# Performance work log

Hardware: AMD Instinct MI355X
Metric: run time of the kernel (lower is better)

## Reference

```python
import jax, jax.numpy as jnp
import numpy as np

B, N, D, L, V, E = 16, 512, 512, 4, 128, 131072
PAD = 127

def setup_inputs() -> dict:
    key = jax.random.key(0)
    ks = jax.random.split(key, 16)
    src_tokens = jax.random.randint(ks[0], (B, N), 0, PAD)  # 0..126, never PAD
    padded_coordinates = jax.random.normal(ks[1], (B, N, 3), dtype=jnp.float32)
    src_distance = jax.random.uniform(ks[2], (B, N, N), dtype=jnp.float32)
    src_edge_type = jax.random.randint(ks[3], (B, N, N), 0, 16)
    edge_index = jax.random.randint(ks[4], (2, E), 0, B * N)
    s = 0.02
    embed_tokens = jax.random.normal(ks[5], (V, D), dtype=jnp.float32) * s
    embed_tokens = embed_tokens.at[PAD].set(0.0)  # nn.Embedding padding_idx row is zero
    vec_proj_w = jax.random.normal(ks[6], (3, D), dtype=jnp.float32) * s
    vec_proj_b = jnp.zeros((D,), dtype=jnp.float32)
    Wq = jax.random.normal(ks[7], (L, D, D), dtype=jnp.float32) * s
    bq = jnp.zeros((L, D), dtype=jnp.float32)
    Wkv = jax.random.normal(ks[8], (L, D, 3 * D), dtype=jnp.float32) * s
    bkv = jnp.zeros((L, 3 * D), dtype=jnp.float32)
    Wvm = jax.random.normal(ks[9], (L, D, D), dtype=jnp.float32) * s
    bvm = jnp.zeros((L, D), dtype=jnp.float32)
    return dict(src_tokens=src_tokens, padded_coordinates=padded_coordinates,
                src_distance=src_distance, src_edge_type=src_edge_type,
                edge_index=edge_index, embed_tokens=embed_tokens,
                vec_proj_w=vec_proj_w, vec_proj_b=vec_proj_b,
                Wq=Wq, bq=bq, Wkv=Wkv, bkv=bkv, Wvm=Wvm, bvm=bvm)

def reference(src_tokens, padded_coordinates, src_distance, src_edge_type,
              edge_index, embed_tokens, vec_proj_w, vec_proj_b,
              Wq, bq, Wkv, bkv, Wvm, bvm):
    padding_mask = src_tokens == PAD                      # [B,N] (all False here)
    x = embed_tokens[src_tokens].reshape(B * N, D)        # [BN,D]
    coord = padded_coordinates.reshape(B * N, 3)          # [BN,3]
    v = coord @ vec_proj_w + vec_proj_b                   # [BN,D]
    row, col = edge_index[0], edge_index[1]               # [E]
    for l in range(L):
        q = x @ Wq[l] + bq[l]                             # [BN,D]
        kv = x @ Wkv[l] + bkv[l]                          # [BN,3D]
        k, v_s, v_v = jnp.split(kv, 3, axis=-1)
        ew = jnp.sum(q[row] * k[col], axis=-1, keepdims=True)   # [E,1] edge score
        msg_s = ew * v_s[col]                             # [E,D]
        msg_v = ew * v_v[col] * v[col]                    # [E,D] gated vector message
        agg_s = jnp.zeros_like(x).at[row].add(msg_s)      # scatter-add to dest nodes
        agg_v = jnp.zeros_like(v).at[row].add(msg_v)
        x = x + agg_s
        v = v + (agg_v @ Wvm[l] + bvm[l])
    out = jnp.where(padding_mask.reshape(-1, 1), 0.0, x).reshape(B, N, D)
    return out, padding_mask
```

## Files before the change

kernel.cpp:

```cpp
#include <hip/hip_runtime.h>
#include <hip/hip_bf16.h>

#define NNODE 8192
#define DIM 512
#define NEDGE 131072
#define NLAYER 4
#define PADIDX 127

typedef float4 f4;
typedef __attribute__((ext_vector_type(8))) short s16x8;
typedef __attribute__((ext_vector_type(4))) float f32x4;

static __device__ __forceinline__ float bf2f(unsigned short h){
  return __uint_as_float(((unsigned int)h) << 16);
}
static __device__ __forceinline__ unsigned short f2bf(float f){
  unsigned int u = __float_as_uint(f);
  u += 0x7FFFu + ((u >> 16) & 1u);
  return (unsigned short)(u >> 16);
}
static __device__ __forceinline__ float blo(unsigned int u){ return __uint_as_float(u << 16); }
static __device__ __forceinline__ float bhi(unsigned int u){ return __uint_as_float(u & 0xFFFF0000u); }
static __device__ __forceinline__ unsigned int pack2(float a, float b){
  return (unsigned int)f2bf(a) | ((unsigned int)f2bf(b) << 16);
}

__global__ void k_detect(const unsigned short* __restrict__ src, int* __restrict__ flag){
  int lane = threadIdx.x;
  float v = bf2f(src[2*lane]);
  float a = fabsf(v);
  bool good = (a > 1e-6f) && (a < 0.5f);
  unsigned long long m = __ballot(good);
  if (lane == 0) *flag = (__popcll(m) >= 32) ? 1 : 0;
}

__global__ void k_convert(const void* __restrict__ src, float* __restrict__ dst, int n,
                          const int* __restrict__ flag){
  int f = *flag;
  int i = blockIdx.x*blockDim.x + threadIdx.x;
  int stride = gridDim.x*blockDim.x;
  if (f){
    const unsigned short* s = (const unsigned short*)src;
    for (; i<n; i+=stride) dst[i] = bf2f(s[i]);
  } else {
    const float* s = (const float*)src;
    for (; i<n; i+=stride) dst[i] = s[i];
  }
}

__global__ void k_convT(const void* __restrict__ src, unsigned short* __restrict__ dst,
                        int C, int dstOff, int dstStride, const int* __restrict__ flag){
  int f = *flag;
  int i = blockIdx.x*blockDim.x + threadIdx.x;
  if (i >= 512*C) return;
  int r = i & 511;
  int c = i >> 9;
  size_t si = (size_t)blockIdx.z*512*C + (size_t)r*C + c;
  unsigned short o;
  if (f) o = ((const unsigned short*)src)[si];
  else   o = f2bf(((const float*)src)[si]);
  dst[(size_t)blockIdx.z*dstStride + (size_t)(dstOff + c)*512 + r] = o;
}

__global__ void k_bias(const void* __restrict__ bq, const void* __restrict__ bkv,
                       float* __restrict__ dst, const int* __restrict__ flag){
  int f = *flag;
  int gid = blockIdx.x*blockDim.x + threadIdx.x;
  if (gid >= NLAYER*2048) return;
  int l = gid >> 11, j = gid & 2047;
  float val;
  if (j < 512)
    val = f ? bf2f(((const unsigned short*)bq)[l*512+j]) : ((const float*)bq)[l*512+j];
  else
    val = f ? bf2f(((const unsigned short*)bkv)[l*1536 + j-512]) : ((const float*)bkv)[l*1536 + j-512];
  dst[gid] = val;
}

__global__ void k_zero_i(int* __restrict__ p, int n){
  int i = blockIdx.x*blockDim.x + threadIdx.x;
  if (i<n) p[i]=0;
}

__global__ void k_count(const int* __restrict__ row, int* __restrict__ counts){
  int e = blockIdx.x*blockDim.x + threadIdx.x;
  if (e<NEDGE) atomicAdd(&counts[row[e]], 1);
}

__global__ __launch_bounds__(1024) void k_scan(const int* __restrict__ counts,
                                               int* __restrict__ offs, int* __restrict__ cursor){
  __shared__ int part[1024];
  int tid = threadIdx.x;
  int local[8]; int s = 0;
  #pragma unroll
  for (int j=0;j<8;j++){ local[j]=s; s += counts[tid*8+j]; }
  part[tid]=s;
  __syncthreads();
  for (int off=1; off<1024; off<<=1){
    int t = (tid>=off) ? part[tid-off] : 0;
    __syncthreads();
    part[tid] += t;
    __syncthreads();
  }
  int base = (tid>0) ? part[tid-1] : 0;
  #pragma unroll
  for (int j=0;j<8;j++){ int o = base + local[j]; offs[tid*8+j]=o; cursor[tid*8+j]=o; }
  if (tid==1023) offs[8192] = part[1023];
}

__global__ void k_fill(const int* __restrict__ ei, int* __restrict__ cursor, int* __restrict__ ecol){
  int e = blockIdx.x*blockDim.x + threadIdx.x;
  if (e<NEDGE){ int p = atomicAdd(&cursor[ei[e]], 1); ecol[p] = ei[NEDGE+e]; }
}

__global__ void k_init(const int* __restrict__ tok, const float* __restrict__ emb,
                       const float* __restrict__ coord, const float* __restrict__ vw,
                       const float* __restrict__ vb, float* __restrict__ x,
                       float* __restrict__ v, unsigned short* __restrict__ xbf){
  int i = blockIdx.x*blockDim.x + threadIdx.x;
  if (i >= NNODE*DIM) return;
  int n = i >> 9, d = i & 511;
  int t = tok[n];
  float xv = emb[(t<<9)|d];
  x[i] = xv;
  xbf[i] = f2bf(xv);
  float c0 = coord[n*3+0], c1 = coord[n*3+1], c2 = coord[n*3+2];
  v[i] = c0*vw[d] + c1*vw[512+d] + c2*vw[1024+d] + vb[d];
}

#define BM 128
#define BN 128
#define BK 64

static __device__ __forceinline__ void gload16(const void* g, void* l){
  __builtin_amdgcn_global_load_lds(
      (const __attribute__((address_space(1))) void*)g,
      (__attribute__((address_space(3))) void*)l, 16, 0, 0);
}

__global__ __launch_bounds__(256) void k_mgemm(const unsigned short* __restrict__ A,
                                               const unsigned short* __restrict__ Bt,
                                               const float* __restrict__ bias,
                                               void* __restrict__ C,
                                               int ldc, int mode){
  __shared__ alignas(16) unsigned short As[BM*BK];
  __shared__ alignas(16) unsigned short Bs[BN*BK];
  int tid  = threadIdx.x;
  int lane = tid & 63;
  int w    = tid >> 6;
  int wr   = (w >> 1) * 64;
  int wc   = (w & 1) * 64;
  int bm   = blockIdx.y * BM;
  int bn   = blockIdx.x * BN;

  f32x4 acc[4][4];
  #pragma unroll
  for (int m=0;m<4;m++)
    #pragma unroll
    for (int n=0;n<4;n++) acc[m][n] = (f32x4){0.f,0.f,0.f,0.f};

  int srow = tid >> 3;
  int sp   = tid & 7;
  char* AsB = (char*)As;
  char* BsB = (char*)Bs;

  for (int kt = 0; kt < 512; kt += BK){
    if (kt) __syncthreads();
    #pragma unroll
    for (int i=0;i<4;i++){
      int row  = i*32 + srow;
      int slot = sp ^ (row & 7);
      gload16((const char*)A + (((size_t)(bm + row)) << 10) + (size_t)((kt + slot*8) << 1),
              AsB + i*4096 + w*1024);
    }
    #pragma unroll
    for (int i=0;i<4;i++){
      int row  = i*32 + srow;
      int slot = sp ^ (row & 7);
      gload16((const char*)Bt + (((size_t)(bn + row)) << 10) + (size_t)((kt + slot*8) << 1),
              BsB + i*4096 + w*1024);
    }
    __syncthreads();

    s16x8 af[4][2], bfr[4][2];
    #pragma unroll
    for (int m=0;m<4;m++){
      int row = wr + m*16 + (lane & 15);
      #pragma unroll
      for (int kk=0;kk<2;kk++){
        int slot = kk*4 + (lane >> 4);
        af[m][kk] = *(const s16x8*)(AsB + row*128 + ((slot ^ (row & 7)) << 4));
      }
    }
    #pragma unroll
    for (int n=0;n<4;n++){
      int row = wc + n*16 + (lane & 15);
      #pragma unroll
      for (int kk=0;kk<2;kk++){
        int slot = kk*4 + (lane >> 4);
        bfr[n][kk] = *(const s16x8*)(BsB + row*128 + ((slot ^ (row & 7)) << 4));
      }
    }
    #pragma unroll
    for (int kk=0;kk<2;kk++)
      #pragma unroll
      for (int m=0;m<4;m++)
        #pragma unroll
        for (int n=0;n<4;n++)
          acc[m][n] = __builtin_amdgcn_mfma_f32_16x16x32_bf16(af[m][kk], bfr[n][kk], acc[m][n], 0, 0, 0);
  }

  int colb = bn + wc + (lane & 15);
  int rowb = bm + wr + ((lane >> 4) << 2);
  float bb[4];
  #pragma unroll
  for (int n=0;n<4;n++) bb[n] = bias[colb + n*16];
  #pragma unroll
  for (int m=0;m<4;m++){
    #pragma unroll
    for (int n=0;n<4;n++){
      #pragma unroll
      for (int j=0;j<4;j++){
        size_t o = (size_t)(rowb + m*16 + j)*ldc + (colb + n*16);
        float val = acc[m][n][j] + bb[n];
        if (mode == 2)      ((unsigned short*)C)[o] = f2bf(val);
        else if (mode == 1) ((float*)C)[o] += val;
        else                ((float*)C)[o] = val;
      }
    }
  }
}

__global__ void k_vvip(unsigned short* __restrict__ qkv, const float* __restrict__ v){
  int gid = blockIdx.x*blockDim.x + threadIdx.x;
  int n = gid >> 6, d8 = (gid & 63) * 8;
  unsigned short* p = qkv + (size_t)n*2048 + 1536 + d8;
  uint4 u = *(uint4*)p;
  f4 v0 = *(const f4*)(v + (size_t)n*512 + d8);
  f4 v1 = *(const f4*)(v + (size_t)n*512 + d8 + 4);
  uint4 o;
  o.x = pack2(blo(u.x)*v0.x, bhi(u.x)*v0.y);
  o.y = pack2(blo(u.y)*v0.z, bhi(u.y)*v0.w);
  o.z = pack2(blo(u.z)*v1.x, bhi(u.z)*v1.y);
  o.w = pack2(blo(u.w)*v1.z, bhi(u.w)*v1.w);
  *(uint4*)p = o;
}

__global__ __launch_bounds__(256) void k_fused(const int* __restrict__ offs,
                                               const int* __restrict__ ecol,
                                               const unsigned short* __restrict__ qkv,
                                               float* __restrict__ x,
                                               unsigned short* __restrict__ xbf,
                                               unsigned short* __restrict__ aggvbf){
  __shared__ unsigned short qs[512];
  __shared__ float ews[64];
  __shared__ int cols[64];
  int n = blockIdx.x, tid = threadIdx.x;
  int beg = offs[n], end = offs[n+1];
  if (tid < 64)
    *(uint4*)&qs[tid*8] = *(const uint4*)(qkv + (size_t)n*2048 + tid*8);
  float a0=0.f, a1=0.f, a2=0.f, a3=0.f;
  int half = tid >> 7;
  int d4 = (tid & 127) * 4;
  size_t srcoff = half ? 1536 : 1024;
  int lane = tid & 63, w = tid >> 6;

  for (int cb = beg; cb < end; cb += 64){
    int cnt = min(64, end - cb);
    __syncthreads();
    for (int j = w; j < cnt; j += 4){
      int c = ecol[cb + j];
      uint4 ku = *(const uint4*)(qkv + (size_t)c*2048 + 512 + lane*8);
      uint4 qu = *(const uint4*)(qs + lane*8);
      float s = blo(qu.x)*blo(ku.x) + bhi(qu.x)*bhi(ku.x)
              + blo(qu.y)*blo(ku.y) + bhi(qu.y)*bhi(ku.y)
              + blo(qu.z)*blo(ku.z) + bhi(qu.z)*bhi(ku.z)
              + blo(qu.w)*blo(ku.w) + bhi(qu.w)*bhi(ku.w);
      #pragma unroll
      for (int o=32;o;o>>=1) s += __shfl_xor(s, o, 64);
      if (lane == 0){ ews[j] = s; cols[j] = c; }
    }
    __syncthreads();
    #pragma unroll 2
    for (int j = 0; j < cnt; j++){
      float wgt = ews[j];
      int c = cols[j];
      uint2 u = *(const uint2*)(qkv + (size_t)c*2048 + srcoff + d4);
      a0 += wgt*blo(u.x); a1 += wgt*bhi(u.x);
      a2 += wgt*blo(u.y); a3 += wgt*bhi(u.y);
    }
  }

  size_t base = (size_t)n*512 + d4;
  if (half == 0){
    f4 xv = *(const f4*)(x + base);
    xv.x += a0; xv.y += a1; xv.z += a2; xv.w += a3;
    *(f4*)(x + base) = xv;
    uint2 o; o.x = pack2(xv.x, xv.y); o.y = pack2(xv.z, xv.w);
    *(uint2*)(xbf + base) = o;
  } else {
    uint2 o; o.x = pack2(a0, a1); o.y = pack2(a2, a3);
    *(uint2*)(aggvbf + base) = o;
  }
}

__global__ void k_out(const int* __restrict__ tok, const float* __restrict__ x,
                      float* __restrict__ out, int out_size){
  int i = blockIdx.x*blockDim.x + threadIdx.x;
  if (i>=out_size) return;
  if (i < NNODE*DIM){
    int n = i>>9;
    out[i] = (tok[n]==PADIDX) ? 0.f : x[i];
  } else {
    int m = i - NNODE*DIM;
    out[i] = (m < NNODE && tok[m]==PADIDX) ? 1.f : 0.f;
  }
}

extern "C" void kernel_launch(void* const* d_in, const int* in_sizes, int n_in,
                              void* d_out, int out_size, void* d_ws, size_t ws_size,
                              hipStream_t stream){
  (void)in_sizes; (void)n_in; (void)ws_size;
  const int*  tok   = (const int*)d_in[0];
  const void* coord = d_in[1];
  const int*  ei    = (const int*)d_in[4];
  const void* emb   = d_in[5];
  const void* vpw   = d_in[6];
  const void* vpb   = d_in[7];
  const void* Wq    = d_in[8];
  const void* bq    = d_in[9];
  const void* Wkv   = d_in[10];
  const void* bkv   = d_in[11];
  const void* Wvm   = d_in[12];
  const void* bvm   = d_in[13];

  char* p = (char*)d_ws;
  auto alloc = [&](size_t nbytes)->char*{ char* r = p; p += (nbytes + 255) & ~(size_t)255; return r; };
  float* x      = (float*)alloc((size_t)NNODE*DIM*4);
  float* v      = (float*)alloc((size_t)NNODE*DIM*4);
  unsigned short* qkv    = (unsigned short*)alloc((size_t)NNODE*2048*2);
  unsigned short* xbf    = (unsigned short*)alloc((size_t)NNODE*DIM*2);
  unsigned short* aggvbf = (unsigned short*)alloc((size_t)NNODE*DIM*2);
  unsigned short* WqkvT  = (unsigned short*)alloc((size_t)NLAYER*2048*DIM*2);
  unsigned short* WvmT   = (unsigned short*)alloc((size_t)NLAYER*DIM*DIM*2);
  float* cEmb   = (float*)alloc((size_t)128*DIM*4);
  float* cCoord = (float*)alloc((size_t)NNODE*3*4);
  float* cVw    = (float*)alloc((size_t)3*DIM*4);
  float* cVb    = (float*)alloc((size_t)DIM*4);
  float* cbqkv  = (float*)alloc((size_t)NLAYER*2048*4);
  float* cbvm   = (float*)alloc((size_t)NLAYER*DIM*4);
  int* counts   = (int*)alloc(8192*4);
  int* offs     = (int*)alloc(8193*4);
  int* cursor   = (int*)alloc(8192*4);
  int* ecol     = (int*)alloc((size_t)NEDGE*4);
  int* flag     = (int*)alloc(4);

  k_detect<<<1,64,0,stream>>>((const unsigned short*)Wq, flag);
  auto conv = [&](const void* s, float* d, int n){
    int blocks = (n+255)/256; if (blocks>8192) blocks=8192;
    k_convert<<<blocks,256,0,stream>>>(s, d, n, flag);
  };
  conv(coord, cCoord, NNODE*3);
  conv(emb,   cEmb,   128*DIM);
  conv(vpw,   cVw,    3*DIM);
  conv(vpb,   cVb,    DIM);
  conv(bvm,   cbvm,   NLAYER*DIM);
  k_bias<<<(NLAYER*2048+255)/256,256,0,stream>>>(bq, bkv, cbqkv, flag);
  k_convT<<<dim3((512*512+255)/256,1,NLAYER),256,0,stream>>>(Wq,  WqkvT, 512,  0,   2048*512, flag);
  k_convT<<<dim3((512*1536+255)/256,1,NLAYER),256,0,stream>>>(Wkv, WqkvT, 1536, 512, 2048*512, flag);
  k_convT<<<dim3((512*512+255)/256,1,NLAYER),256,0,stream>>>(Wvm, WvmT,  512,  0,   512*512,  flag);

  k_zero_i<<<32,256,0,stream>>>(counts, 8192);
  k_count<<<NEDGE/256,256,0,stream>>>(ei, counts);
  k_scan<<<1,1024,0,stream>>>(counts, offs, cursor);
  k_fill<<<NEDGE/256,256,0,stream>>>(ei, cursor, ecol);

  k_init<<<(NNODE*DIM)/256,256,0,stream>>>(tok, cEmb, cCoord, cVw, cVb, x, v, xbf);

  for (int l=0;l<NLAYER;l++){
    const unsigned short* WqkvT_l = WqkvT + (size_t)l*2048*DIM;
    const unsigned short* WvmT_l  = WvmT  + (size_t)l*DIM*DIM;
    const float* bqkv_l = cbqkv + (size_t)l*2048;
    const float* bvm_l  = cbvm  + (size_t)l*DIM;
    k_mgemm<<<dim3(2048/BN, NNODE/BM),256,0,stream>>>(xbf, WqkvT_l, bqkv_l, qkv, 2048, 2);
    k_vvip<<<NNODE*64/256,256,0,stream>>>(qkv, v);
    k_fused<<<NNODE,256,0,stream>>>(offs, ecol, qkv, x, xbf, aggvbf);
    k_mgemm<<<dim3(DIM/BN, NNODE/BM),256,0,stream>>>(aggvbf, WvmT_l, bvm_l, v, 512, 1);
  }

  int ob = (out_size+255)/256;
  k_out<<<ob,256,0,stream>>>(tok, x, (float*)d_out, out_size);
}
```

Before: 688.5 us.

## Fuse v-gating into QKV GEMM epilogue and widen aggregation loads

Removes the separate k_vvip kernel by multiplying the v_v columns by the vector feature v inside the QKV GEMM epilogue (new mode 3). It also restructures the aggregation kernel so each thread loads 8 bf16 values per edge with two wave pairs splitting edges by parity, then reduces the halves through shared memory. The aim is to save a kernel launch and a full read/write pass over the v_v slice, and to halve the number of gather instructions. In exchange the epilogue does an extra strided global read of v, and the aggregation kernel gains an extra sync and shared-memory reduction. Gating now multiplies in fp32 before rounding to bf16 instead of after, a slight numeric difference.

```diff
diff --git a/kernel.cpp b/kernel.cpp
--- a/kernel.cpp
+++ b/kernel.cpp
@@ -140,6 +140,7 @@
 __global__ __launch_bounds__(256) void k_mgemm(const unsigned short* __restrict__ A,
                                                const unsigned short* __restrict__ Bt,
                                                const float* __restrict__ bias,
+                                               const float* __restrict__ vgate,
                                                void* __restrict__ C,
                                                int ldc, int mode){
   __shared__ alignas(16) unsigned short As[BM*BK];
@@ -211,6 +212,7 @@
 
   int colb = bn + wc + (lane & 15);
   int rowb = bm + wr + ((lane >> 4) << 2);
+  bool gated = (mode == 3) && (bn >= 1536);
   float bb[4];
   #pragma unroll
   for (int n=0;n<4;n++) bb[n] = bias[colb + n*16];
@@ -220,29 +222,18 @@
     for (int n=0;n<4;n++){
       #pragma unroll
       for (int j=0;j<4;j++){
-        size_t o = (size_t)(rowb + m*16 + j)*ldc + (colb + n*16);
+        int row = rowb + m*16 + j;
+        int col = colb + n*16;
+        size_t o = (size_t)row*ldc + col;
         float val = acc[m][n][j] + bb[n];
-        if (mode == 2)      ((unsigned short*)C)[o] = f2bf(val);
-        else if (mode == 1) ((float*)C)[o] += val;
-        else                ((float*)C)[o] = val;
+        if (mode >= 2){
+          if (gated) val *= vgate[(size_t)row*512 + (col - 1536)];
+          ((unsigned short*)C)[o] = f2bf(val);
+        } else if (mode == 1) ((float*)C)[o] += val;
+        else                  ((float*)C)[o] = val;
       }
     }
   }
-}
-
-__global__ void k_vvip(unsigned short* __restrict__ qkv, const float* __restrict__ v){
-  int gid = blockIdx.x*blockDim.x + threadIdx.x;
-  int n = gid >> 6, d8 = (gid & 63) * 8;
-  unsigned short* p = qkv + (size_t)n*2048 + 1536 + d8;
-  uint4 u = *(uint4*)p;
-  f4 v0 = *(const f4*)(v + (size_t)n*512 + d8);
-  f4 v1 = *(const f4*)(v + (size_t)n*512 + d8 + 4);
-  uint4 o;
-  o.x = pack2(blo(u.x)*v0.x, bhi(u.x)*v0.y);
-  o.y = pack2(blo(u.y)*v0.z, bhi(u.y)*v0.w);
-  o.z = pack2(blo(u.z)*v1.x, bhi(u.z)*v1.y);
-  o.w = pack2(blo(u.w)*v1.z, bhi(u.w)*v1.w);
-  *(uint4*)p = o;
 }
 
 __global__ __launch_bounds__(256) void k_fused(const int* __restrict__ offs,
@@ -254,23 +245,28 @@
   __shared__ unsigned short qs[512];
   __shared__ float ews[64];
   __shared__ int cols[64];
+  __shared__ float red[2][64][9];
   int n = blockIdx.x, tid = threadIdx.x;
   int beg = offs[n], end = offs[n+1];
   if (tid < 64)
     *(uint4*)&qs[tid*8] = *(const uint4*)(qkv + (size_t)n*2048 + tid*8);
-  float a0=0.f, a1=0.f, a2=0.f, a3=0.f;
-  int half = tid >> 7;
-  int d4 = (tid & 127) * 4;
-  size_t srcoff = half ? 1536 : 1024;
-  int lane = tid & 63, w = tid >> 6;
+
+  int sub  = tid >> 6;
+  int lane = tid & 63;
+  int d8   = lane * 8;
+  size_t suboff = (sub & 1) ? 1536 : 1024;
+  int par  = sub >> 1;
+  float a[8];
+  #pragma unroll
+  for (int k=0;k<8;k++) a[k] = 0.f;
 
   for (int cb = beg; cb < end; cb += 64){
     int cnt = min(64, end - cb);
     __syncthreads();
-    for (int j = w; j < cnt; j += 4){
+    for (int j = sub; j < cnt; j += 4){
       int c = ecol[cb + j];
-      uint4 ku = *(const uint4*)(qkv + (size_t)c*2048 + 512 + lane*8);
-      uint4 qu = *(const uint4*)(qs + lane*8);
+      uint4 ku = *(const uint4*)(qkv + (size_t)c*2048 + 512 + d8);
+      uint4 qu = *(const uint4*)(qs + d8);
       float s = blo(qu.x)*blo(ku.x) + bhi(qu.x)*bhi(ku.x)
               + blo(qu.y)*blo(ku.y) + bhi(qu.y)*bhi(ku.y)
               + blo(qu.z)*blo(ku.z) + bhi(qu.z)*bhi(ku.z)
@@ -281,25 +277,44 @@
     }
     __syncthreads();
     #pragma unroll 2
-    for (int j = 0; j < cnt; j++){
+    for (int j = par; j < cnt; j += 2){
       float wgt = ews[j];
       int c = cols[j];
-      uint2 u = *(const uint2*)(qkv + (size_t)c*2048 + srcoff + d4);
-      a0 += wgt*blo(u.x); a1 += wgt*bhi(u.x);
-      a2 += wgt*blo(u.y); a3 += wgt*bhi(u.y);
-    }
-  }
-
-  size_t base = (size_t)n*512 + d4;
-  if (half == 0){
-    f4 xv = *(const f4*)(x + base);
-    xv.x += a0; xv.y += a1; xv.z += a2; xv.w += a3;
-    *(f4*)(x + base) = xv;
-    uint2 o; o.x = pack2(xv.x, xv.y); o.y = pack2(xv.z, xv.w);
-    *(uint2*)(xbf + base) = o;
-  } else {
-    uint2 o; o.x = pack2(a0, a1); o.y = pack2(a2, a3);
-    *(uint2*)(aggvbf + base) = o;
+      uint4 u = *(const uint4*)(qkv + (size_t)c*2048 + suboff + d8);
+      a[0] += wgt*blo(u.x); a[1] += wgt*bhi(u.x);
+      a[2] += wgt*blo(u.y); a[3] += wgt*bhi(u.y);
+      a[4] += wgt*blo(u.z); a[5] += wgt*bhi(u.z);
+      a[6] += wgt*blo(u.w); a[7] += wgt*bhi(u.w);
+    }
+  }
+
+  __syncthreads();
+  if (par == 1){
+    #pragma unroll
+    for (int k=0;k<8;k++) red[sub & 1][lane][k] = a[k];
+  }
+  __syncthreads();
+  if (par == 0){
+    #pragma unroll
+    for (int k=0;k<8;k++) a[k] += red[sub & 1][lane][k];
+    size_t base = (size_t)n*512 + d8;
+    if (sub == 0){
+      f4 x0 = *(const f4*)(x + base);
+      f4 x1 = *(const f4*)(x + base + 4);
+      x0.x += a[0]; x0.y += a[1]; x0.z += a[2]; x0.w += a[3];
+      x1.x += a[4]; x1.y += a[5]; x1.z += a[6]; x1.w += a[7];
+      *(f4*)(x + base)     = x0;
+      *(f4*)(x + base + 4) = x1;
+      uint4 o;
+      o.x = pack2(x0.x, x0.y); o.y = pack2(x0.z, x0.w);
+      o.z = pack2(x1.x, x1.y); o.w = pack2(x1.z, x1.w);
+      *(uint4*)(xbf + base) = o;
+    } else {
+      uint4 o;
+      o.x = pack2(a[0], a[1]); o.y = pack2(a[2], a[3]);
+      o.z = pack2(a[4], a[5]); o.w = pack2(a[6], a[7]);
+      *(uint4*)(aggvbf + base) = o;
+    }
   }
 }
 
@@ -381,10 +396,9 @@
     const unsigned short* WvmT_l  = WvmT  + (size_t)l*DIM*DIM;
     const float* bqkv_l = cbqkv + (size_t)l*2048;
     const float* bvm_l  = cbvm  + (size_t)l*DIM;
-    k_mgemm<<<dim3(2048/BN, NNODE/BM),256,0,stream>>>(xbf, WqkvT_l, bqkv_l, qkv, 2048, 2);
-    k_vvip<<<NNODE*64/256,256,0,stream>>>(qkv, v);
+    k_mgemm<<<dim3(2048/BN, NNODE/BM),256,0,stream>>>(xbf, WqkvT_l, bqkv_l, v, qkv, 2048, 3);
     k_fused<<<NNODE,256,0,stream>>>(offs, ecol, qkv, x, xbf, aggvbf);
-    k_mgemm<<<dim3(DIM/BN, NNODE/BM),256,0,stream>>>(aggvbf, WvmT_l, bvm_l, v, 512, 1);
+    k_mgemm<<<dim3(DIM/BN, NNODE/BM),256,0,stream>>>(aggvbf, WvmT_l, bvm_l, nullptr, v, 512, 1);
   }
 
   int ob = (out_size+255)/256;
```

Measured after the change: 782.5 us. 1.14x slower.

## Double-buffer GEMM LDS tiles and fold input conversion into init kernel

Applied to the files above, without the earlier changes.

The bf16 MFMA GEMM now keeps two LDS buffers and issues the global-to-LDS loads for the next K tile before computing the current one, so there is one barrier per iteration instead of two and load latency overlaps with compute. Separately, the per-tensor dtype conversion kernels for embedding, coordinates and the vector-projection weight and bias are removed, and k_init reads the raw inputs directly, branching on the detected dtype flag. This removes four small launches and their scratch buffers. LDS use per block doubles to 64 KB, which may lower occupancy.

```diff
diff --git a/kernel.cpp b/kernel.cpp
--- a/kernel.cpp
+++ b/kernel.cpp
@@ -112,19 +112,39 @@
   if (e<NEDGE){ int p = atomicAdd(&cursor[ei[e]], 1); ecol[p] = ei[NEDGE+e]; }
 }
 
-__global__ void k_init(const int* __restrict__ tok, const float* __restrict__ emb,
-                       const float* __restrict__ coord, const float* __restrict__ vw,
-                       const float* __restrict__ vb, float* __restrict__ x,
-                       float* __restrict__ v, unsigned short* __restrict__ xbf){
+__global__ void k_init(const int* __restrict__ tok, const void* __restrict__ emb,
+                       const void* __restrict__ coord, const void* __restrict__ vw,
+                       const void* __restrict__ vb, const int* __restrict__ flag,
+                       float* __restrict__ x, float* __restrict__ v,
+                       unsigned short* __restrict__ xbf){
+  int f = *flag;
   int i = blockIdx.x*blockDim.x + threadIdx.x;
   if (i >= NNODE*DIM) return;
   int n = i >> 9, d = i & 511;
   int t = tok[n];
-  float xv = emb[(t<<9)|d];
+  float xv, c0, c1, c2, w0, w1, w2, bb;
+  if (f){
+    const unsigned short* e = (const unsigned short*)emb;
+    const unsigned short* c = (const unsigned short*)coord;
+    const unsigned short* wv = (const unsigned short*)vw;
+    const unsigned short* bv = (const unsigned short*)vb;
+    xv = bf2f(e[(t<<9)|d]);
+    c0 = bf2f(c[n*3+0]); c1 = bf2f(c[n*3+1]); c2 = bf2f(c[n*3+2]);
+    w0 = bf2f(wv[d]); w1 = bf2f(wv[512+d]); w2 = bf2f(wv[1024+d]);
+    bb = bf2f(bv[d]);
+  } else {
+    const float* e = (const float*)emb;
+    const float* c = (const float*)coord;
+    const float* wv = (const float*)vw;
+    const float* bv = (const float*)vb;
+    xv = e[(t<<9)|d];
+    c0 = c[n*3+0]; c1 = c[n*3+1]; c2 = c[n*3+2];
+    w0 = wv[d]; w1 = wv[512+d]; w2 = wv[1024+d];
+    bb = bv[d];
+  }
   x[i] = xv;
   xbf[i] = f2bf(xv);
-  float c0 = coord[n*3+0], c1 = coord[n*3+1], c2 = coord[n*3+2];
-  v[i] = c0*vw[d] + c1*vw[512+d] + c2*vw[1024+d] + vb[d];
+  v[i] = c0*w0 + c1*w1 + c2*w2 + bb;
 }
 
 #define BM 128
@@ -142,8 +162,8 @@
                                                const float* __restrict__ bias,
                                                void* __restrict__ C,
                                                int ldc, int mode){
-  __shared__ alignas(16) unsigned short As[BM*BK];
-  __shared__ alignas(16) unsigned short Bs[BN*BK];
+  __shared__ alignas(16) unsigned short As[2][BM*BK];
+  __shared__ alignas(16) unsigned short Bs[2][BN*BK];
   int tid  = threadIdx.x;
   int lane = tid & 63;
   int w    = tid >> 6;
@@ -160,11 +180,10 @@
 
   int srow = tid >> 3;
   int sp   = tid & 7;
-  char* AsB = (char*)As;
-  char* BsB = (char*)Bs;
-
-  for (int kt = 0; kt < 512; kt += BK){
-    if (kt) __syncthreads();
+
+  auto STAGE = [&](int b, int kt){
+    char* AsB = (char*)As[b];
+    char* BsB = (char*)Bs[b];
     #pragma unroll
     for (int i=0;i<4;i++){
       int row  = i*32 + srow;
@@ -179,7 +198,15 @@
       gload16((const char*)Bt + (((size_t)(bn + row)) << 10) + (size_t)((kt + slot*8) << 1),
               BsB + i*4096 + w*1024);
     }
-    __syncthreads();
+  };
+
+  STAGE(0, 0);
+  __syncthreads();
+
+  for (int it = 0; it < 8; ++it){
+    if (it < 7) STAGE((it+1)&1, (it+1)*BK);
+    const char* AsB = (const char*)As[it&1];
+    const char* BsB = (const char*)Bs[it&1];
 
     s16x8 af[4][2], bfr[4][2];
     #pragma unroll
@@ -207,6 +234,8 @@
         #pragma unroll
         for (int n=0;n<4;n++)
           acc[m][n] = __builtin_amdgcn_mfma_f32_16x16x32_bf16(af[m][kk], bfr[n][kk], acc[m][n], 0, 0, 0);
+
+    if (it < 7) __syncthreads();
   }
 
   int colb = bn + wc + (lane & 15);
@@ -342,10 +371,6 @@
   unsigned short* aggvbf = (unsigned short*)alloc((size_t)NNODE*DIM*2);
   unsigned short* WqkvT  = (unsigned short*)alloc((size_t)NLAYER*2048*DIM*2);
   unsigned short* WvmT   = (unsigned short*)alloc((size_t)NLAYER*DIM*DIM*2);
-  float* cEmb   = (float*)alloc((size_t)128*DIM*4);
-  float* cCoord = (float*)alloc((size_t)NNODE*3*4);
-  float* cVw    = (float*)alloc((size_t)3*DIM*4);
-  float* cVb    = (float*)alloc((size_t)DIM*4);
   float* cbqkv  = (float*)alloc((size_t)NLAYER*2048*4);
   float* cbvm   = (float*)alloc((size_t)NLAYER*DIM*4);
   int* counts   = (int*)alloc(8192*4);
@@ -355,15 +380,7 @@
   int* flag     = (int*)alloc(4);
 
   k_detect<<<1,64,0,stream>>>((const unsigned short*)Wq, flag);
-  auto conv = [&](const void* s, float* d, int n){
-    int blocks = (n+255)/256; if (blocks>8192) blocks=8192;
-    k_convert<<<blocks,256,0,stream>>>(s, d, n, flag);
-  };
-  conv(coord, cCoord, NNODE*3);
-  conv(emb,   cEmb,   128*DIM);
-  conv(vpw,   cVw,    3*DIM);
-  conv(vpb,   cVb,    DIM);
-  conv(bvm,   cbvm,   NLAYER*DIM);
+  k_convert<<<8,256,0,stream>>>(bvm, cbvm, NLAYER*DIM, flag);
   k_bias<<<(NLAYER*2048+255)/256,256,0,stream>>>(bq, bkv, cbqkv, flag);
   k_convT<<<dim3((512*512+255)/256,1,NLAYER),256,0,stream>>>(Wq,  WqkvT, 512,  0,   2048*512, flag);
   k_convT<<<dim3((512*1536+255)/256,1,NLAYER),256,0,stream>>>(Wkv, WqkvT, 1536, 512, 2048*512, flag);
@@ -374,7 +391,7 @@
   k_scan<<<1,1024,0,stream>>>(counts, offs, cursor);
   k_fill<<<NEDGE/256,256,0,stream>>>(ei, cursor, ecol);
 
-  k_init<<<(NNODE*DIM)/256,256,0,stream>>>(tok, cEmb, cCoord, cVw, cVb, x, v, xbf);
+  k_init<<<(NNODE*DIM)/256,256,0,stream>>>(tok, emb, coord, vpw, vpb, flag, x, v, xbf);
 
   for (int l=0;l<NLAYER;l++){
     const unsigned short* WqkvT_l = WqkvT + (size_t)l*2048*DIM;
```

Result: no change. 697.5 us (+1.3%).
